# Kernel optimization log

Hardware: AMD Instinct MI355X
Metric: run time of the kernel (lower is better)

The kernel has to match this reference:

```python
import jax, jax.numpy as jnp
import numpy as np

B, T, C = 4, 2048, 1024
H, D = 16, 64          # n_head, head_size; H*D == C
FF = 4 * C             # compute_layer_scaling * n_embed
EPS = 1e-5


def layernorm(x, g, b):
    mu = jnp.mean(x, axis=-1, keepdims=True)
    var = jnp.var(x, axis=-1, keepdims=True)
    return (x - mu) * jax.lax.rsqrt(var + EPS) * g + b


def setup_inputs() -> dict:
    key = jax.random.key(0)
    ks = jax.random.split(key, 12)
    s_c = 1.0 / np.sqrt(C)
    s_ff = 1.0 / np.sqrt(FF)
    return {
        "x": jax.random.normal(ks[0], (B, T, C), dtype=jnp.float32),
        # per-head Q/K/V weights, stacked: [H, C, D] (Linear with bias=False)
        "Wq": jax.random.normal(ks[1], (H, C, D), dtype=jnp.float32) * s_c,
        "Wk": jax.random.normal(ks[2], (H, C, D), dtype=jnp.float32) * s_c,
        "Wv": jax.random.normal(ks[3], (H, C, D), dtype=jnp.float32) * s_c,
        "Wproj": jax.random.normal(ks[4], (C, C), dtype=jnp.float32) * s_c,
        "bproj": jnp.zeros((C,), dtype=jnp.float32),
        "W1": jax.random.normal(ks[5], (C, FF), dtype=jnp.float32) * s_c,
        "b1": jnp.zeros((FF,), dtype=jnp.float32),
        "W2": jax.random.normal(ks[6], (FF, FF), dtype=jnp.float32) * s_ff,
        "b2": jnp.zeros((FF,), dtype=jnp.float32),
        "W3": jax.random.normal(ks[7], (FF, C), dtype=jnp.float32) * s_ff,
        "b3": jnp.zeros((C,), dtype=jnp.float32),
        "ln1_g": jnp.ones((C,), dtype=jnp.float32),
        "ln1_b": jnp.zeros((C,), dtype=jnp.float32),
        "ln2_g": jnp.ones((C,), dtype=jnp.float32),
        "ln2_b": jnp.zeros((C,), dtype=jnp.float32),
    }


def reference(x, Wq, Wk, Wv, Wproj, bproj, W1, b1, W2, b2, W3, b3,
              ln1_g, ln1_b, ln2_g, ln2_b):
    # --- multi-head causal self-attention (pre-LN) ---
    h = layernorm(x, ln1_g, ln1_b)
    q = jnp.einsum("btc,hcd->bhtd", h, Wq)
    k = jnp.einsum("btc,hcd->bhtd", h, Wk)
    v = jnp.einsum("btc,hcd->bhtd", h, Wv)
    # NOTE: original scales by n_embed**-0.5 (C from x.shape), not head_size
    scores = jnp.einsum("bhtd,bhsd->bhts", q, k) * (C ** -0.5)
    causal = jnp.tril(jnp.ones((T, T), dtype=bool))
    scores = jnp.where(causal, scores, -jnp.inf)
    wei = jax.nn.softmax(scores, axis=-1)          # dropout p=0 -> identity
    attn = jnp.einsum("bhts,bhsd->bhtd", wei, v)
    attn = attn.transpose(0, 2, 1, 3).reshape(B, T, C)  # concat heads
    x = x + attn @ Wproj + bproj
    # --- feed-forward (pre-LN): C -> FF -> relu -> FF -> relu -> C ---
    h2 = layernorm(x, ln2_g, ln2_b)
    h2 = jax.nn.relu(h2 @ W1 + b1)
    h2 = jax.nn.relu(h2 @ W2 + b2)
    x = x + h2 @ W3 + b3
    return x
```

## Files before the change

### kernel.cpp

```cpp
#include <hip/hip_runtime.h>

typedef __bf16 bf16;
typedef bf16  bf16x8 __attribute__((ext_vector_type(8)));
typedef bf16  bf16x4 __attribute__((ext_vector_type(4)));
typedef float f32x4  __attribute__((ext_vector_type(4)));

#define T_SEQ 2048

__device__ __forceinline__ void gload_lds16(const bf16* g, bf16* l) {
    __builtin_amdgcn_global_load_lds(
        (const __attribute__((address_space(1))) unsigned int*)g,
        (__attribute__((address_space(3))) unsigned int*)l,
        16, 0, 0);
}

#define VMCNT(n) asm volatile("s_waitcnt vmcnt(" #n ")" ::: "memory")
#define BAR() do { asm volatile("" ::: "memory"); __builtin_amdgcn_s_barrier(); \
                   asm volatile("" ::: "memory"); } while (0)

__global__ __launch_bounds__(256) void transpose_f32_bf16(
    const float* __restrict__ in, bf16* __restrict__ out, int R, int Cc, int ldo)
{
    __shared__ float tile[32][33];
    const int bx = blockIdx.x * 32;
    const int by = blockIdx.y * 32;
    const long bi = (long)blockIdx.z * R * Cc;
    const long bo = (long)blockIdx.z * Cc * ldo;
    const int tx = threadIdx.x, ty = threadIdx.y;
#pragma unroll
    for (int i = 0; i < 4; ++i)
        tile[ty + i * 8][tx] = in[bi + (long)(by + ty + i * 8) * Cc + bx + tx];
    __syncthreads();
#pragma unroll
    for (int i = 0; i < 4; ++i)
        out[bo + (long)(bx + ty + i * 8) * ldo + by + tx] = (bf16)tile[tx][ty + i * 8];
}

__global__ __launch_bounds__(256) void ln_kernel(
    const float* __restrict__ x, const float* __restrict__ g,
    const float* __restrict__ bb, bf16* __restrict__ out)
{
    const long row = blockIdx.x;
    const int tid = threadIdx.x;
    const float4 v = ((const float4*)(x + row * 1024))[tid];
    float s  = v.x + v.y + v.z + v.w;
    float s2 = v.x * v.x + v.y * v.y + v.z * v.z + v.w * v.w;
#pragma unroll
    for (int off = 32; off >= 1; off >>= 1) {
        s  += __shfl_xor(s,  off, 64);
        s2 += __shfl_xor(s2, off, 64);
    }
    __shared__ float red[8];
    const int wid = tid >> 6;
    if ((tid & 63) == 0) { red[wid] = s; red[4 + wid] = s2; }
    __syncthreads();
    s  = red[0] + red[1] + red[2] + red[3];
    s2 = red[4] + red[5] + red[6] + red[7];
    const float mu   = s * (1.f / 1024.f);
    const float rstd = rsqrtf(s2 * (1.f / 1024.f) - mu * mu + 1e-5f);
    const float4 gv = ((const float4*)g)[tid];
    const float4 bv = ((const float4*)bb)[tid];
    bf16x4 ov;
    ov[0] = (bf16)((v.x - mu) * rstd * gv.x + bv.x);
    ov[1] = (bf16)((v.y - mu) * rstd * gv.y + bv.y);
    ov[2] = (bf16)((v.z - mu) * rstd * gv.z + bv.z);
    ov[3] = (bf16)((v.w - mu) * rstd * gv.w + bv.w);
    *(bf16x4*)(out + row * 1024 + tid * 4) = ov;
}

#define LOADA(BUFP, QM) do {                                                   \
    const char* ab_ = (BUFP) + (size_t)((wr * 64 + (QM) * 128 + fr) * 128);    \
    _Pragma("unroll") for (int m_ = 0; m_ < 4; ++m_) {                         \
        af[m_][0] = *(const bf16x8*)(ab_ + m_ * 2048 + so0);                   \
        af[m_][1] = *(const bf16x8*)(ab_ + m_ * 2048 + so1); } } while (0)

#define LOADB(BUFP, QN) do {                                                   \
    const char* bb_ = (BUFP) + (size_t)((wc * 32 + (QN) * 128 + fr) * 128);    \
    _Pragma("unroll") for (int n_ = 0; n_ < 2; ++n_) {                         \
        bfv[n_][0] = *(const bf16x8*)(bb_ + n_ * 2048 + so0);                  \
        bfv[n_][1] = *(const bf16x8*)(bb_ + n_ * 2048 + so1); } } while (0)

#define MMA(ACC) do { __builtin_amdgcn_s_setprio(1);                           \
    _Pragma("unroll") for (int m_ = 0; m_ < 4; ++m_)                           \
    _Pragma("unroll") for (int n_ = 0; n_ < 2; ++n_) {                         \
        ACC[m_][n_] = __builtin_amdgcn_mfma_f32_16x16x32_bf16(                 \
            af[m_][0], bfv[n_][0], ACC[m_][n_], 0, 0, 0);                      \
        ACC[m_][n_] = __builtin_amdgcn_mfma_f32_16x16x32_bf16(                 \
            af[m_][1], bfv[n_][1], ACC[m_][n_], 0, 0, 0); }                    \
    __builtin_amdgcn_s_setprio(0); } while (0)

#define TILE_BODY(PRE) do {                                                    \
    const char* abuf = cAs + ((size_t)cur << 15);                              \
    const char* bbuf = cBs + ((size_t)cur << 15);                              \
    const long kn = (long)(k + 1) * 64;                                        \
    LOADA(abuf, 0);                                                            \
    LOADB(bbuf, 0);                                                            \
    if (PRE) { stageA(nxt, 0, kn); VMCNT(4); } else { VMCNT(2); }              \
    BAR(); MMA(a00); BAR();                                                    \
    LOADB(bbuf, 1);                                                            \
    if (PRE) { stageB(nxt, 0, kn); VMCNT(4); } else { VMCNT(0); }              \
    BAR(); MMA(a01); BAR();                                                    \
    LOADA(abuf, 1);                                                            \
    if (PRE) { stageB(nxt, 1, kn); }                                           \
    BAR(); MMA(a11); BAR();                                                    \
    LOADB(bbuf, 0);                                                            \
    if (PRE) { stageA(nxt, 1, kn); VMCNT(4); }                                 \
    BAR(); MMA(a10); BAR(); } while (0)

template <int MODE>
__global__ __launch_bounds__(512, 2) void gemm256(
    const bf16* __restrict__ A, const bf16* __restrict__ Bt,
    const float* __restrict__ bias, const float* __restrict__ resid,
    void* __restrict__ outp, int M, int N, int K, int nbn)
{
    extern __shared__ __align__(16) char smem[];
    char* cAs = smem;
    char* cBs = smem + 65536;

    const int tid = threadIdx.x;
    const int wid = tid >> 6, lane = tid & 63;
    const int wr = wid >> 2, wc = wid & 3;
    const int fr = lane & 15, fq = lane >> 4;

    const int nwg = gridDim.x;
    const int cpx = nwg >> 3;
    const int b0  = blockIdx.x;
    const int bid = (b0 & 7) * cpx + (b0 >> 3);
    const long bm = bid / nbn, bn = bid % nbn;
    const long bmrow = bm * 256, bnrow = bn * 256;

    const int srow0 = wid * 8 + (lane >> 3);
    const int sslot = (lane & 7) ^ (lane >> 3);
    auto stageA = [&](int buf, int h, long kt) {
        const bf16* g = A + (size_t)(bmrow + h * 128 + srow0) * K + kt + sslot * 8;
        char* l = cAs + ((size_t)buf << 15) + h * 16384 + (size_t)wid * 1024;
        gload_lds16(g, (bf16*)l);
        gload_lds16(g + (size_t)64 * K, (bf16*)(l + 8192));
    };
    auto stageB = [&](int buf, int h, long kt) {
        const bf16* g = Bt + (size_t)(bnrow + h * 128 + srow0) * K + kt + sslot * 8;
        char* l = cBs + ((size_t)buf << 15) + h * 16384 + (size_t)wid * 1024;
        gload_lds16(g, (bf16*)l);
        gload_lds16(g + (size_t)64 * K, (bf16*)(l + 8192));
    };

    const int sx  = fr & 7;
    const int so0 = ((fq) ^ sx) * 16;
    const int so1 = ((4 + fq) ^ sx) * 16;

    bf16x8 af[4][2], bfv[2][2];
    f32x4 a00[4][2], a01[4][2], a11[4][2], a10[4][2];
#pragma unroll
    for (int m = 0; m < 4; ++m)
#pragma unroll
        for (int n = 0; n < 2; ++n) {
            a00[m][n] = {0.f, 0.f, 0.f, 0.f}; a01[m][n] = {0.f, 0.f, 0.f, 0.f};
            a11[m][n] = {0.f, 0.f, 0.f, 0.f}; a10[m][n] = {0.f, 0.f, 0.f, 0.f};
        }

    stageA(0, 0, 0); stageB(0, 0, 0); stageB(0, 1, 0); stageA(0, 1, 0);
    VMCNT(4);
    BAR();

    const int NT = K >> 6;
    int cur = 0, nxt = 1;
    int k = 0;
    for (; k < NT - 1; ++k) {
        cur = k & 1; nxt = cur ^ 1;
        TILE_BODY(true);
    }
    cur = k & 1; nxt = cur ^ 1;
    TILE_BODY(false);

    auto writeQ = [&](f32x4 (&acc)[4][2], int QM, int QN) {
#pragma unroll
        for (int m = 0; m < 4; ++m) {
            const long row0 = bmrow + wr * 64 + QM * 128 + m * 16 + fq * 4;
#pragma unroll
            for (int n = 0; n < 2; ++n) {
                const long col = bnrow + wc * 32 + QN * 128 + n * 16 + fr;
                const float bv = (MODE == 0) ? 0.f : bias[col];
#pragma unroll
                for (int j = 0; j < 4; ++j) {
                    const long row = row0 + j;
                    float v = acc[m][n][j] + bv;
                    if (MODE == 1) v = fmaxf(v, 0.f);
                    if (MODE == 2) {
                        v += resid[row * N + col];
                        ((float*)outp)[row * N + col] = v;
                    } else {
                        ((bf16*)outp)[row * N + col] = (bf16)v;
                    }
                }
            }
        }
    };
    writeQ(a00, 0, 0); writeQ(a01, 0, 1); writeQ(a11, 1, 1); writeQ(a10, 1, 0);
}

#define TILE_BODY_N(PRE, LAST) do {                                            \
    const char* abuf = cAs + ((size_t)cur << 15);                              \
    const char* bbuf = cBs + ((size_t)cur << 14);                              \
    const long kn = (long)(k + 1) * 64;                                        \
    LOADA(abuf, 0);                                                            \
    LOADB(bbuf, 0);                                                            \
    if (PRE) { stageA(nxt, 0, kn); VMCNT(2); } else { VMCNT(0); }              \
    BAR(); MMA(aq0); BAR();                                                    \
    LOADA(abuf, 1);                                                            \
    if (PRE) { stageB(nxt, kn); stageA(nxt, 1, kn); VMCNT(2); }                \
    if (!LAST) { BAR(); }                                                      \
    MMA(aq1);                                                                  \
    if (!LAST) { BAR(); } } while (0)

template <int MODE>
__global__ __launch_bounds__(512, 2) void gemm256n(
    const bf16* __restrict__ A, const bf16* __restrict__ Bt,
    const float* __restrict__ bias, const float* __restrict__ resid,
    void* __restrict__ outp, int M, int N, int K, int nbn)
{
    extern __shared__ __align__(16) char smem[];
    char* cAs = smem;
    char* cBs = smem + 65536;

    const int tid = threadIdx.x;
    const int wid = tid >> 6, lane = tid & 63;
    const int wr = wid >> 2, wc = wid & 3;
    const int fr = lane & 15, fq = lane >> 4;

    const int nwg = gridDim.x;
    const int cpx = nwg >> 3;
    const int b0  = blockIdx.x;
    const int bid = (b0 & 7) * cpx + (b0 >> 3);
    const long bm = bid / nbn, bn = bid % nbn;
    const long bmrow = bm * 256, bnrow = bn * 128;

    const int srow0 = wid * 8 + (lane >> 3);
    const int sslot = (lane & 7) ^ (lane >> 3);
    auto stageA = [&](int buf, int h, long kt) {
        const bf16* g = A + (size_t)(bmrow + h * 128 + srow0) * K + kt + sslot * 8;
        char* l = cAs + ((size_t)buf << 15) + h * 16384 + (size_t)wid * 1024;
        gload_lds16(g, (bf16*)l);
        gload_lds16(g + (size_t)64 * K, (bf16*)(l + 8192));
    };
    auto stageB = [&](int buf, long kt) {
        const bf16* g = Bt + (size_t)(bnrow + srow0) * K + kt + sslot * 8;
        char* l = cBs + ((size_t)buf << 14) + (size_t)wid * 1024;
        gload_lds16(g, (bf16*)l);
        gload_lds16(g + (size_t)64 * K, (bf16*)(l + 8192));
    };

    const int sx  = fr & 7;
    const int so0 = ((fq) ^ sx) * 16;
    const int so1 = ((4 + fq) ^ sx) * 16;

    bf16x8 af[4][2], bfv[2][2];
    f32x4 aq0[4][2], aq1[4][2];
#pragma unroll
    for (int m = 0; m < 4; ++m)
#pragma unroll
        for (int n = 0; n < 2; ++n) {
            aq0[m][n] = {0.f, 0.f, 0.f, 0.f};
            aq1[m][n] = {0.f, 0.f, 0.f, 0.f};
        }

    stageA(0, 0, 0); stageB(0, 0); stageA(0, 1, 0);
    VMCNT(2);
    BAR();

    const int NT = K >> 6;
    int cur = 0, nxt = 1;
    int k = 0;
    for (; k < NT - 1; ++k) {
        cur = k & 1; nxt = cur ^ 1;
        TILE_BODY_N(true, false);
    }
    cur = k & 1; nxt = cur ^ 1;
    TILE_BODY_N(false, true);

    auto writeQ = [&](f32x4 (&acc)[4][2], int QM) {
#pragma unroll
        for (int m = 0; m < 4; ++m) {
            const long row0 = bmrow + wr * 64 + QM * 128 + m * 16 + fq * 4;
#pragma unroll
            for (int n = 0; n < 2; ++n) {
                const long col = bnrow + wc * 32 + n * 16 + fr;
                const float bv = (MODE == 0) ? 0.f : bias[col];
#pragma unroll
                for (int j = 0; j < 4; ++j) {
                    const long row = row0 + j;
                    float v = acc[m][n][j] + bv;
                    if (MODE == 1) v = fmaxf(v, 0.f);
                    if (MODE == 2) {
                        v += resid[row * N + col];
                        ((float*)outp)[row * N + col] = v;
                    } else {
                        ((bf16*)outp)[row * N + col] = (bf16)v;
                    }
                }
            }
        }
    };
    writeQ(aq0, 0); writeQ(aq1, 1);
}

__device__ __forceinline__ void attn_step(
    const bf16* __restrict__ Ks, const bf16* __restrict__ Vt,
    bf16* __restrict__ Pp, const bf16x8* qf,
    f32x4* o, f32x4& o_l, float* mj, const bf16x8 onesf,
    int fr, int fq, int qloc, bool diag)
{
    f32x4 s[4];
#pragma unroll
    for (int n = 0; n < 4; ++n) s[n] = {0.f, 0.f, 0.f, 0.f};
#pragma unroll
    for (int n = 0; n < 4; ++n) {
        const int t  = n * 16 + fr;
        const int sw = ((t ^ (t >> 3)) & 7) << 4;
#pragma unroll
        for (int kk = 0; kk < 2; ++kk) {
            const bf16x8 kf = *(const bf16x8*)((const char*)Ks + t * 128
                                               + ((kk * 64 + fq * 16) ^ sw));
            s[n] = __builtin_amdgcn_mfma_f32_16x16x32_bf16(qf[kk], kf, s[n], 0, 0, 0);
        }
    }
    float v[4][4], mxj[4];
#pragma unroll
    for (int j = 0; j < 4; ++j) {
        const int qg = qloc + fq * 4 + j;
        v[0][j] = s[0][j] * 0.03125f;
        v[1][j] = s[1][j] * 0.03125f;
        v[2][j] = s[2][j] * 0.03125f;
        v[3][j] = s[3][j] * 0.03125f;
        if (diag) {
            if (fr      > qg) v[0][j] = -1e30f;
            if (16 + fr > qg) v[1][j] = -1e30f;
            if (32 + fr > qg) v[2][j] = -1e30f;
            if (48 + fr > qg) v[3][j] = -1e30f;
        }
        float mx = fmaxf(fmaxf(v[0][j], v[1][j]), fmaxf(v[2][j], v[3][j]));
#pragma unroll
        for (int off = 1; off <= 8; off <<= 1) mx = fmaxf(mx, __shfl_xor(mx, off, 16));
        mxj[j] = mx;
    }
    float need = mxj[0] - mj[0];
    need = fmaxf(need, mxj[1] - mj[1]);
    need = fmaxf(need, mxj[2] - mj[2]);
    need = fmaxf(need, mxj[3] - mj[3]);
    if (__any(need > 8.f)) {
#pragma unroll
        for (int j = 0; j < 4; ++j) {
            const float mn   = fmaxf(mj[j], mxj[j]);
            const float corr = __expf(mj[j] - mn);
            mj[j] = mn;
#pragma unroll
            for (int nd = 0; nd < 4; ++nd) o[nd][j] *= corr;
            o_l[j] *= corr;
        }
    }
#pragma unroll
    for (int j = 0; j < 4; ++j) {
        bf16* prow = Pp + (fq * 4 + j) * 72;
        prow[fr]      = (bf16)__expf(v[0][j] - mj[j]);
        prow[16 + fr] = (bf16)__expf(v[1][j] - mj[j]);
        prow[32 + fr] = (bf16)__expf(v[2][j] - mj[j]);
        prow[48 + fr] = (bf16)__expf(v[3][j] - mj[j]);
    }
    asm volatile("s_waitcnt lgkmcnt(0)" ::: "memory");
    __builtin_amdgcn_sched_barrier(0);
    const bf16x8 pf0 = *(const bf16x8*)(Pp + fr * 72 + fq * 8);
    const bf16x8 pf1 = *(const bf16x8*)(Pp + fr * 72 + 32 + fq * 8);
#pragma unroll
    for (int nd = 0; nd < 4; ++nd) {
        const int dd = nd * 16 + fr;
        const int sw = ((dd ^ (dd >> 3)) & 7) << 4;
        const bf16x8 vf0 = *(const bf16x8*)((const char*)Vt + dd * 128 + ((fq * 16) ^ sw));
        const bf16x8 vf1 = *(const bf16x8*)((const char*)Vt + dd * 128 + ((64 + fq * 16) ^ sw));
        o[nd] = __builtin_amdgcn_mfma_f32_16x16x32_bf16(pf0, vf0, o[nd], 0, 0, 0);
        o[nd] = __builtin_amdgcn_mfma_f32_16x16x32_bf16(pf1, vf1, o[nd], 0, 0, 0);
    }
    o_l = __builtin_amdgcn_mfma_f32_16x16x32_bf16(pf0, onesf, o_l, 0, 0, 0);
    o_l = __builtin_amdgcn_mfma_f32_16x16x32_bf16(pf1, onesf, o_l, 0, 0, 0);
}

__global__ __launch_bounds__(256) void attn_kernel(
    const bf16* __restrict__ qkv, bf16* __restrict__ out)
{
    const int pair = blockIdx.x;
    const int h = blockIdx.y, b = blockIdx.z;
    const int tid = threadIdx.x, wid = tid >> 6, lane = tid & 63;
    const int fr = lane & 15, fq = lane >> 4;
    const int jA = pair, jB = 31 - pair;
    const bf16* base = qkv + ((long)b * T_SEQ) * 3072 + h * 64;

    __shared__ __align__(16) bf16 Ks[64 * 64];
    __shared__ __align__(16) bf16 Vt[64 * 64];
    __shared__ __align__(16) bf16 Plds[2][4][16 * 72];

    const int qrA = jA * 64 + wid * 16 + fr;
    const int qrB = jB * 64 + wid * 16 + fr;
    bf16x8 qfA[2], qfB[2];
#pragma unroll
    for (int kk = 0; kk < 2; ++kk) {
        qfA[kk] = *(const bf16x8*)(base + (long)qrA * 3072 + kk * 32 + fq * 8);
        qfB[kk] = *(const bf16x8*)(base + (long)qrB * 3072 + kk * 32 + fq * 8);
    }

    bf16x8 onesf;
    {
        const bf16 ov = (fr == 0) ? (bf16)1.f : (bf16)0.f;
#pragma unroll
        for (int e = 0; e < 8; ++e) onesf[e] = ov;
    }

    f32x4 oA[4], oB[4], olA, olB;
    float mA[4], mB[4];
#pragma unroll
    for (int nd = 0; nd < 4; ++nd) { oA[nd] = {0.f, 0.f, 0.f, 0.f}; oB[nd] = {0.f, 0.f, 0.f, 0.f}; }
    olA = {0.f, 0.f, 0.f, 0.f}; olB = {0.f, 0.f, 0.f, 0.f};
#pragma unroll
    for (int j = 0; j < 4; ++j) { mA[j] = -1e30f; mB[j] = -1e30f; }

    const int t_p0 = wid * 16 + (lane >> 3);
    const int t_p1 = t_p0 + 8;
    const int kcb0 = ((lane & 7) * 16) ^ (((t_p0 ^ (t_p0 >> 3)) & 7) << 4);
    const int kcb1 = ((lane & 7) * 16) ^ (((t_p1 ^ (t_p1 >> 3)) & 7) << 4);
    bf16* lK0 = &Ks[(wid * 2) * 512];
    bf16* lK1 = &Ks[(wid * 2 + 1) * 512];
    const int vtok = tid >> 3;
    const int vd0  = (tid & 7) * 8;

    bf16* PA = &Plds[0][wid][0];
    bf16* PB = &Plds[1][wid][0];

    const int nch = jB + 1;
    for (int c = 0; c < nch; ++c) {
        const int s0 = c * 64;
        const bf16* vsrc = base + (long)(s0 + vtok) * 3072 + 2048 + vd0;
        const bf16x8 vv0 = *(const bf16x8*)vsrc;
        const bf16x8 vv1 = *(const bf16x8*)(vsrc + 32l * 3072);
        __syncthreads();
        gload_lds16(base + (long)(s0 + t_p0) * 3072 + 1024 + (kcb0 >> 1), lK0);
        gload_lds16(base + (long)(s0 + t_p1) * 3072 + 1024 + (kcb1 >> 1), lK1);
#pragma unroll
        for (int e = 0; e < 8; ++e) {
            const int d  = vd0 + e;
            const int sw = ((d ^ (d >> 3)) & 7) << 4;
            *(bf16*)((char*)Vt + ((d * 128 + vtok * 2) ^ sw))        = vv0[e];
            *(bf16*)((char*)Vt + ((d * 128 + (vtok + 32) * 2) ^ sw)) = vv1[e];
        }
        __syncthreads();
        if (c <= jA)
            attn_step(Ks, Vt, PA, qfA, oA, olA, mA, onesf, fr, fq, wid * 16, c == jA);
        attn_step(Ks, Vt, PB, qfB, oB, olB, mB, onesf, fr, fq, wid * 16, c == jB);
    }

#pragma unroll
    for (int j = 0; j < 4; ++j) {
        const float lA = __shfl(olA[j], lane & 48, 64);
        const float lB = __shfl(olB[j], lane & 48, 64);
        const float rA = 1.f / lA, rB = 1.f / lB;
        const long rowA = (long)b * T_SEQ + jA * 64 + wid * 16 + fq * 4 + j;
        const long rowB = (long)b * T_SEQ + jB * 64 + wid * 16 + fq * 4 + j;
#pragma unroll
        for (int nd = 0; nd < 4; ++nd) {
            out[rowA * 1024 + h * 64 + nd * 16 + fr] = (bf16)(oA[nd][j] * rA);
            out[rowB * 1024 + h * 64 + nd * 16 + fr] = (bf16)(oB[nd][j] * rB);
        }
    }
}

extern "C" void kernel_launch(void* const* d_in, const int* in_sizes, int n_in,
                              void* d_out, int out_size, void* d_ws, size_t ws_size,
                              hipStream_t stream)
{
    const float* x     = (const float*)d_in[0];
    const float* Wq    = (const float*)d_in[1];
    const float* Wk    = (const float*)d_in[2];
    const float* Wv    = (const float*)d_in[3];
    const float* Wproj = (const float*)d_in[4];
    const float* bproj = (const float*)d_in[5];
    const float* W1    = (const float*)d_in[6];
    const float* b1    = (const float*)d_in[7];
    const float* W2    = (const float*)d_in[8];
    const float* b2    = (const float*)d_in[9];
    const float* W3    = (const float*)d_in[10];
    const float* b3    = (const float*)d_in[11];
    const float* ln1g  = (const float*)d_in[12];
    const float* ln1b  = (const float*)d_in[13];
    const float* ln2g  = (const float*)d_in[14];
    const float* ln2b  = (const float*)d_in[15];

    char* ws = (char*)d_ws;
    size_t off = 0;
    auto alloc = [&](size_t bytes) {
        void* p = ws + off;
        off += (bytes + 255) & ~(size_t)255;
        return p;
    };
    bf16* Wqkv_t  = (bf16*)alloc(3072ul * 1024 * 2);
    bf16* Wproj_t = (bf16*)alloc(1024ul * 1024 * 2);
    bf16* W1_t    = (bf16*)alloc(4096ul * 1024 * 2);
    bf16* W2_t    = (bf16*)alloc(4096ul * 4096 * 2);
    bf16* W3_t    = (bf16*)alloc(1024ul * 4096 * 2);
    bf16* hbuf    = (bf16*)alloc(8192ul * 1024 * 2);
    float* x1     = (float*)alloc(8192ul * 1024 * 4);
    bf16* a1      = (bf16*)alloc(8192ul * 4096 * 2);
    char* R1      = (char*)alloc(8192ul * 4096 * 2);
    bf16* qkvb    = (bf16*)R1;
    bf16* attnb   = (bf16*)(R1 + 8192ul * 3072 * 2);
    bf16* a2      = (bf16*)R1;

    hipFuncSetAttribute(reinterpret_cast<const void*>(&gemm256<1>),
                        hipFuncAttributeMaxDynamicSharedMemorySize, 131072);
    hipFuncSetAttribute(reinterpret_cast<const void*>(&gemm256n<0>),
                        hipFuncAttributeMaxDynamicSharedMemorySize, 98304);
    hipFuncSetAttribute(reinterpret_cast<const void*>(&gemm256n<2>),
                        hipFuncAttributeMaxDynamicSharedMemorySize, 98304);

    const dim3 tb(32, 8);
    transpose_f32_bf16<<<dim3(2, 32, 16), tb, 0, stream>>>(Wq, Wqkv_t,                1024, 64, 1024);
    transpose_f32_bf16<<<dim3(2, 32, 16), tb, 0, stream>>>(Wk, Wqkv_t + 1024l * 1024, 1024, 64, 1024);
    transpose_f32_bf16<<<dim3(2, 32, 16), tb, 0, stream>>>(Wv, Wqkv_t + 2048l * 1024, 1024, 64, 1024);
    transpose_f32_bf16<<<dim3(32, 32, 1),   tb, 0, stream>>>(Wproj, Wproj_t, 1024, 1024, 1024);
    transpose_f32_bf16<<<dim3(128, 32, 1),  tb, 0, stream>>>(W1, W1_t, 1024, 4096, 1024);
    transpose_f32_bf16<<<dim3(128, 128, 1), tb, 0, stream>>>(W2, W2_t, 4096, 4096, 4096);
    transpose_f32_bf16<<<dim3(32, 128, 1),  tb, 0, stream>>>(W3, W3_t, 4096, 1024, 4096);

    ln_kernel<<<8192, 256, 0, stream>>>(x, ln1g, ln1b, hbuf);
    gemm256n<0><<<768, 512, 98304, stream>>>(hbuf, Wqkv_t, nullptr, nullptr, qkvb,
                                             8192, 3072, 1024, 24);
    attn_kernel<<<dim3(16, 16, 4), 256, 0, stream>>>(qkvb, attnb);
    gemm256n<2><<<256, 512, 98304, stream>>>(attnb, Wproj_t, bproj, x, x1,
                                             8192, 1024, 1024, 8);
    ln_kernel<<<8192, 256, 0, stream>>>(x1, ln2g, ln2b, hbuf);
    gemm256<1><<<512, 512, 131072, stream>>>(hbuf, W1_t, b1, nullptr, a1,
                                             8192, 4096, 1024, 16);
    gemm256<1><<<512, 512, 131072, stream>>>(a1, W2_t, b2, nullptr, a2,
                                             8192, 4096, 4096, 16);
    gemm256n<2><<<256, 512, 98304, stream>>>(a2, W3_t, b3, x1, (float*)d_out,
                                             8192, 1024, 4096, 8);
}
```

Before: 704.7 us.

## Pre-transpose V and double-buffer attention K/V; issue GEMM prefetches earlier

Adds a bf16 transpose kernel that writes V in [d, token] layout into a spare buffer. The attention kernel can then stage both K and V directly into LDS with async global->LDS loads, double-buffered across chunks, replacing the per-element register scatter of V and the two syncthreads per chunk. Both GEMM tile bodies now issue all next-tile stage loads at the start of the tile with adjusted vmcnt waits, so memory latency overlaps more MFMA work. The cost is an extra kernel launch and an extra pass over V in global memory, plus more LDS in attention. The shared P buffer is now reused by both query blocks in place of two separate buffers.

```diff
diff --git a/kernel.cpp b/kernel.cpp
--- a/kernel.cpp
+++ b/kernel.cpp
@@ -34,6 +34,22 @@
 #pragma unroll
     for (int i = 0; i < 4; ++i)
         out[bo + (long)(bx + ty + i * 8) * ldo + by + tx] = (bf16)tile[tx][ty + i * 8];
+}
+
+__global__ __launch_bounds__(256) void transpose_bf16(
+    const bf16* __restrict__ in, bf16* __restrict__ out, int ldi, int ldo)
+{
+    __shared__ bf16 tile[32][33];
+    const int bx = blockIdx.x * 32;
+    const int by = blockIdx.y * 32;
+    const int tx = threadIdx.x, ty = threadIdx.y;
+#pragma unroll
+    for (int i = 0; i < 4; ++i)
+        tile[ty + i * 8][tx] = in[(long)(by + ty + i * 8) * ldi + bx + tx];
+    __syncthreads();
+#pragma unroll
+    for (int i = 0; i < 4; ++i)
+        out[(long)(bx + ty + i * 8) * ldo + by + tx] = tile[tx][ty + i * 8];
 }
 
 __global__ __launch_bounds__(256) void ln_kernel(
@@ -95,16 +111,17 @@
     const long kn = (long)(k + 1) * 64;                                        \
     LOADA(abuf, 0);                                                            \
     LOADB(bbuf, 0);                                                            \
-    if (PRE) { stageA(nxt, 0, kn); VMCNT(4); } else { VMCNT(2); }              \
+    if (PRE) { stageA(nxt, 0, kn); stageB(nxt, 0, kn);                         \
+               stageB(nxt, 1, kn); stageA(nxt, 1, kn); VMCNT(10); }            \
+    else     { VMCNT(2); }                                                     \
     BAR(); MMA(a00); BAR();                                                    \
     LOADB(bbuf, 1);                                                            \
-    if (PRE) { stageB(nxt, 0, kn); VMCNT(4); } else { VMCNT(0); }              \
+    if (PRE) { VMCNT(8); } else { VMCNT(0); }                                  \
     BAR(); MMA(a01); BAR();                                                    \
     LOADA(abuf, 1);                                                            \
-    if (PRE) { stageB(nxt, 1, kn); }                                           \
     BAR(); MMA(a11); BAR();                                                    \
     LOADB(bbuf, 0);                                                            \
-    if (PRE) { stageA(nxt, 1, kn); VMCNT(4); }                                 \
+    if (PRE) { VMCNT(4); }                                                     \
     BAR(); MMA(a10); BAR(); } while (0)
 
 template <int MODE>
@@ -204,10 +221,12 @@
     const long kn = (long)(k + 1) * 64;                                        \
     LOADA(abuf, 0);                                                            \
     LOADB(bbuf, 0);                                                            \
-    if (PRE) { stageA(nxt, 0, kn); VMCNT(2); } else { VMCNT(0); }              \
+    if (PRE) { stageA(nxt, 0, kn); stageB(nxt, kn); stageA(nxt, 1, kn);        \
+               VMCNT(6); }                                                     \
+    else     { VMCNT(0); }                                                     \
     BAR(); MMA(aq0); BAR();                                                    \
     LOADA(abuf, 1);                                                            \
-    if (PRE) { stageB(nxt, kn); stageA(nxt, 1, kn); VMCNT(2); }                \
+    if (PRE) { VMCNT(2); }                                                     \
     if (!LAST) { BAR(); }                                                      \
     MMA(aq1);                                                                  \
     if (!LAST) { BAR(); } } while (0)
@@ -383,26 +402,29 @@
 }
 
 __global__ __launch_bounds__(256) void attn_kernel(
-    const bf16* __restrict__ qkv, bf16* __restrict__ out)
+    const bf16* __restrict__ qkv, const bf16* __restrict__ vt,
+    bf16* __restrict__ out)
 {
     const int pair = blockIdx.x;
     const int h = blockIdx.y, b = blockIdx.z;
     const int tid = threadIdx.x, wid = tid >> 6, lane = tid & 63;
     const int fr = lane & 15, fq = lane >> 4;
     const int jA = pair, jB = 31 - pair;
-    const bf16* base = qkv + ((long)b * T_SEQ) * 3072 + h * 64;
-
-    __shared__ __align__(16) bf16 Ks[64 * 64];
-    __shared__ __align__(16) bf16 Vt[64 * 64];
-    __shared__ __align__(16) bf16 Plds[2][4][16 * 72];
+    const bf16* baseQ = qkv + ((long)b * T_SEQ) * 3072 + h * 64;
+    const bf16* baseK = baseQ + 1024;
+    const bf16* baseV = vt + (long)(h * 64) * 8192 + (long)b * T_SEQ;
+
+    __shared__ __align__(16) bf16 Ks[2][64 * 64];
+    __shared__ __align__(16) bf16 Vs[2][64 * 64];
+    __shared__ __align__(16) bf16 Plds[4][16 * 72];
 
     const int qrA = jA * 64 + wid * 16 + fr;
     const int qrB = jB * 64 + wid * 16 + fr;
     bf16x8 qfA[2], qfB[2];
 #pragma unroll
     for (int kk = 0; kk < 2; ++kk) {
-        qfA[kk] = *(const bf16x8*)(base + (long)qrA * 3072 + kk * 32 + fq * 8);
-        qfB[kk] = *(const bf16x8*)(base + (long)qrB * 3072 + kk * 32 + fq * 8);
+        qfA[kk] = *(const bf16x8*)(baseQ + (long)qrA * 3072 + kk * 32 + fq * 8);
+        qfB[kk] = *(const bf16x8*)(baseQ + (long)qrB * 3072 + kk * 32 + fq * 8);
     }
 
     bf16x8 onesf;
@@ -424,34 +446,28 @@
     const int t_p1 = t_p0 + 8;
     const int kcb0 = ((lane & 7) * 16) ^ (((t_p0 ^ (t_p0 >> 3)) & 7) << 4);
     const int kcb1 = ((lane & 7) * 16) ^ (((t_p1 ^ (t_p1 >> 3)) & 7) << 4);
-    bf16* lK0 = &Ks[(wid * 2) * 512];
-    bf16* lK1 = &Ks[(wid * 2 + 1) * 512];
-    const int vtok = tid >> 3;
-    const int vd0  = (tid & 7) * 8;
-
-    bf16* PA = &Plds[0][wid][0];
-    bf16* PB = &Plds[1][wid][0];
+
+    bf16* P = &Plds[wid][0];
+
+    auto stage = [&](int buf, int c) {
+        const long s0 = (long)c * 64;
+        gload_lds16(baseK + (s0 + t_p0) * 3072 + (kcb0 >> 1), &Ks[buf][(wid * 2) * 512]);
+        gload_lds16(baseK + (s0 + t_p1) * 3072 + (kcb1 >> 1), &Ks[buf][(wid * 2 + 1) * 512]);
+        gload_lds16(baseV + (long)t_p0 * 8192 + s0 + (kcb0 >> 1), &Vs[buf][(wid * 2) * 512]);
+        gload_lds16(baseV + (long)t_p1 * 8192 + s0 + (kcb1 >> 1), &Vs[buf][(wid * 2 + 1) * 512]);
+    };
 
     const int nch = jB + 1;
+    stage(0, 0);
     for (int c = 0; c < nch; ++c) {
-        const int s0 = c * 64;
-        const bf16* vsrc = base + (long)(s0 + vtok) * 3072 + 2048 + vd0;
-        const bf16x8 vv0 = *(const bf16x8*)vsrc;
-        const bf16x8 vv1 = *(const bf16x8*)(vsrc + 32l * 3072);
-        __syncthreads();
-        gload_lds16(base + (long)(s0 + t_p0) * 3072 + 1024 + (kcb0 >> 1), lK0);
-        gload_lds16(base + (long)(s0 + t_p1) * 3072 + 1024 + (kcb1 >> 1), lK1);
-#pragma unroll
-        for (int e = 0; e < 8; ++e) {
-            const int d  = vd0 + e;
-            const int sw = ((d ^ (d >> 3)) & 7) << 4;
-            *(bf16*)((char*)Vt + ((d * 128 + vtok * 2) ^ sw))        = vv0[e];
-            *(bf16*)((char*)Vt + ((d * 128 + (vtok + 32) * 2) ^ sw)) = vv1[e];
-        }
-        __syncthreads();
+        const int cur = c & 1;
+        if (c + 1 < nch) { stage(cur ^ 1, c + 1); VMCNT(4); }
+        else             { VMCNT(0); }
+        BAR();
         if (c <= jA)
-            attn_step(Ks, Vt, PA, qfA, oA, olA, mA, onesf, fr, fq, wid * 16, c == jA);
-        attn_step(Ks, Vt, PB, qfB, oB, olB, mB, onesf, fr, fq, wid * 16, c == jB);
+            attn_step(Ks[cur], Vs[cur], P, qfA, oA, olA, mA, onesf, fr, fq, wid * 16, c == jA);
+        attn_step(Ks[cur], Vs[cur], P, qfB, oB, olB, mB, onesf, fr, fq, wid * 16, c == jB);
+        BAR();
     }
 
 #pragma unroll
@@ -509,6 +525,7 @@
     bf16* qkvb    = (bf16*)R1;
     bf16* attnb   = (bf16*)(R1 + 8192ul * 3072 * 2);
     bf16* a2      = (bf16*)R1;
+    bf16* vt      = a1;
 
     hipFuncSetAttribute(reinterpret_cast<const void*>(&gemm256<1>),
                         hipFuncAttributeMaxDynamicSharedMemorySize, 131072);
@@ -529,7 +546,8 @@
     ln_kernel<<<8192, 256, 0, stream>>>(x, ln1g, ln1b, hbuf);
     gemm256n<0><<<768, 512, 98304, stream>>>(hbuf, Wqkv_t, nullptr, nullptr, qkvb,
                                              8192, 3072, 1024, 24);
-    attn_kernel<<<dim3(16, 16, 4), 256, 0, stream>>>(qkvb, attnb);
+    transpose_bf16<<<dim3(32, 256), tb, 0, stream>>>(qkvb + 2048, vt, 3072, 8192);
+    attn_kernel<<<dim3(16, 16, 4), 256, 0, stream>>>(qkvb, vt, attnb);
     gemm256n<2><<<256, 512, 98304, stream>>>(attnb, Wproj_t, bproj, x, x1,
                                              8192, 1024, 1024, 8);
     ln_kernel<<<8192, 256, 0, stream>>>(x1, ln2g, ln2b, hbuf);
```

Result: no change. 717.8 us (+1.9%).
